# Optimization experiments

Hardware: AMD Instinct MI355X
Metric: run time of the kernel (lower is better)

The kernel has to match this reference:

```python
import jax, jax.numpy as jnp
import numpy as np

B, N, M, D, F, H = 8, 512, 512, 512, 512, 8
D_H, F_H = D // H, F // H


def setup_inputs() -> dict:
    key = jax.random.key(0)
    ks = jax.random.split(key, 7)
    X = jax.random.normal(ks[0], (B, N, D), dtype=jnp.float32)
    V = jax.random.normal(ks[1], (B, M, F), dtype=jnp.float32)
    # learned parameters, init normal(0, 0.02) as in the torch module
    W_Q_1 = 0.02 * jax.random.normal(ks[2], (H, N, D_H, D_H), dtype=jnp.float32)
    W_Q_2 = 0.02 * jax.random.normal(ks[3], (H, N, M, D_H), dtype=jnp.float32)
    W_V = 0.02 * jax.random.normal(ks[4], (H, F_H, F_H), dtype=jnp.float32)
    O_w = 0.02 * jax.random.normal(ks[5], (F, F), dtype=jnp.float32)
    O_b = jnp.zeros((F,), dtype=jnp.float32)
    return {"X": X, "V": V, "W_Q_1": W_Q_1, "W_Q_2": W_Q_2,
            "W_V": W_V, "O_w": O_w, "O_b": O_b}


def reference(X, V, W_Q_1, W_Q_2, W_V, O_w, O_b):
    b, n, d = X.shape
    _, m, f = V.shape
    Xh = X.reshape(b, n, H, d // H)      # [B,N,H,D_H]
    Vh = V.reshape(b, m, H, f // H)      # [B,M,H,F_H]
    # 'hndd' repeats d within one operand -> diagonal of W_Q_1's last two dims
    # (faithful to torch.einsum semantics): per-position per-channel scale.
    Q_1 = jnp.einsum('bnhd,hndd->bhnd', Xh, W_Q_1)
    Q_1 = jax.nn.gelu(Q_1, approximate=False)  # torch nn.GELU default = exact erf
    Q_2 = jnp.einsum('bhnd,hnmd->bhnm', Q_1, W_Q_2)  # synthesized attention logits
    A = jax.nn.softmax(Q_2, axis=3)                  # softmax over M
    # 'hff' likewise takes the diagonal of W_V -> per-head channel scale fused
    # with the attention-weighted value aggregation.
    Y = jnp.einsum('bhnm,bmhf,hff->bnhf', A, Vh, W_V)
    Y = Y.reshape(b, n, f)
    return Y @ O_w.T + O_b
```

## Files before the change

### kernel.cpp

```cpp
#include <hip/hip_runtime.h>
#include <cstdint>

#define B_ 8
#define N_ 512
#define M_ 512
#define D_ 512
#define F_ 512
#define H_ 8
#define DH_ 64
#define FH_ 64

template <int CTRL>
__device__ __forceinline__ float dpp_add(float x) {
    int y = __builtin_amdgcn_update_dpp(0, __float_as_int(x), CTRL, 0xf, 0xf, true);
    return x + __int_as_float(y);
}

__global__ __launch_bounds__(256, 4) void syn_k_attn(const float* __restrict__ X,
                                                     const float* __restrict__ W1,
                                                     const float* __restrict__ W2,
                                                     float* __restrict__ A) {
    int hn = blockIdx.x;
    int h = hn >> 9, n = hn & 511;
    int t = threadIdx.x;
    int wave = t >> 6, lane = t & 63;
    __shared__ float q1s[8 * 68];
    __shared__ float logits[8 * 520];

    {
        int d = t & 63;
        int b0 = t >> 6;
        float w = W1[(size_t)hn * (DH_ * DH_) + d * (DH_ + 1)];
        #pragma unroll
        for (int i = 0; i < 2; ++i) {
            int bi = b0 + i * 4;
            float x = X[((size_t)(bi * N_ + n)) * D_ + h * DH_ + d];
            float v = x * w;
            q1s[bi * 68 + d] = 0.5f * v * (1.0f + erff(v * 0.70710678118654752440f));
        }
    }
    __syncthreads();

    int mr = lane >> 3, c = lane & 7;
    float4 qa[8], qb[8];
    #pragma unroll
    for (int b = 0; b < 8; ++b) {
        qa[b] = *(const float4*)&q1s[b * 68 + c * 8];
        qb[b] = *(const float4*)&q1s[b * 68 + c * 8 + 4];
    }

    const float* w2 = W2 + (size_t)hn * ((size_t)M_ * DH_);
    #pragma unroll 4
    for (int g = 0; g < 16; ++g) {
        int m = (wave + g * 4) * 8 + mr;
        const float* wr = w2 + (size_t)m * DH_ + c * 8;
        float4 wa = *(const float4*)wr;
        float4 wb = *(const float4*)(wr + 4);
        float acc[8];
        #pragma unroll
        for (int b = 0; b < 8; ++b) {
            float a0 = wa.x * qa[b].x + wa.y * qa[b].y + wa.z * qa[b].z + wa.w * qa[b].w
                     + wb.x * qb[b].x + wb.y * qb[b].y + wb.z * qb[b].z + wb.w * qb[b].w;
            a0 = dpp_add<0xB1>(a0);
            a0 = dpp_add<0x4E>(a0);
            a0 = dpp_add<0x124>(a0);
            acc[b] = a0;
        }
        float lo = c == 0 ? acc[0] : c == 1 ? acc[1] : c == 2 ? acc[2] : acc[3];
        float hi = c == 0 ? acc[4] : c == 1 ? acc[5] : c == 2 ? acc[6] : acc[7];
        if (c < 4) {
            logits[c * 520 + m] = lo;
            logits[(c + 4) * 520 + m] = hi;
        }
    }
    __syncthreads();

    for (int bb = wave; bb < 8; bb += 4) {
        const float* lrow = &logits[bb * 520 + lane * 8];
        float4 va = *(const float4*)lrow;
        float4 vb = *(const float4*)(lrow + 4);
        float v[8] = {va.x, va.y, va.z, va.w, vb.x, vb.y, vb.z, vb.w};
        float mx = v[0];
        #pragma unroll
        for (int i = 1; i < 8; ++i) mx = fmaxf(mx, v[i]);
        #pragma unroll
        for (int s = 1; s < 64; s <<= 1) mx = fmaxf(mx, __shfl_xor(mx, s));
        float e[8]; float sum = 0.f;
        #pragma unroll
        for (int i = 0; i < 8; ++i) { e[i] = expf(v[i] - mx); sum += e[i]; }
        #pragma unroll
        for (int s = 1; s < 64; s <<= 1) sum += __shfl_xor(sum, s);
        float inv = 1.0f / sum;
        float* outp = A + ((size_t)(bb * H_ + h) * N_ + n) * M_ + lane * 8;
        float4 o0 = make_float4(e[0] * inv, e[1] * inv, e[2] * inv, e[3] * inv);
        float4 o1 = make_float4(e[4] * inv, e[5] * inv, e[6] * inv, e[7] * inv);
        *(float4*)outp = o0;
        *(float4*)(outp + 4) = o1;
    }
}


__global__ __launch_bounds__(256) void syn_k_pv(const float* __restrict__ A,
                                                const float* __restrict__ V,
                                                const float* __restrict__ WV,
                                                float* __restrict__ Y) {
    int bh = blockIdx.y;
    int b = bh >> 3, h = bh & 7;
    int n0 = blockIdx.x * 64;
    int t = threadIdx.x;
    int tx = t & 15, ty = t >> 4;
    __shared__ float Alds[64 * 64];
    __shared__ float Vlds[64 * 64];
    float acc[4][4] = {};
    const float* Abase = A + ((size_t)bh * N_ + n0) * M_;
    const float* Vbase = V + (size_t)b * ((size_t)M_ * F_) + h * FH_;
    int kk = tx * 4;
    for (int m0 = 0; m0 < M_; m0 += 64) {
        #pragma unroll
        for (int it = 0; it < 4; ++it) {
            int r = ty + it * 16;
            float4 a4 = *(const float4*)(Abase + (size_t)r * M_ + m0 + kk);
            int slot = ((r >> 2) ^ tx) & 15;
            float* p = &Alds[kk * 64 + slot * 4 + (r & 3)];
            p[0] = a4.x; p[64] = a4.y; p[128] = a4.z; p[192] = a4.w;
            float4 v4 = *(const float4*)(Vbase + (size_t)(m0 + r) * F_ + kk);
            *(float4*)&Vlds[r * 64 + kk] = v4;
        }
        __syncthreads();
        #pragma unroll 2
        for (int k4 = 0; k4 < 16; ++k4) {
            int sa = ((ty ^ k4) & 15) * 4;
            #pragma unroll
            for (int kj = 0; kj < 4; ++kj) {
                int k = k4 * 4 + kj;
                float4 a4 = *(const float4*)&Alds[k * 64 + sa];
                float4 v4 = *(const float4*)&Vlds[k * 64 + tx * 4];
                float ar[4] = {a4.x, a4.y, a4.z, a4.w};
                float vr[4] = {v4.x, v4.y, v4.z, v4.w};
                #pragma unroll
                for (int i = 0; i < 4; ++i)
                    #pragma unroll
                    for (int j = 0; j < 4; ++j)
                        acc[i][j] += ar[i] * vr[j];
            }
        }
        __syncthreads();
    }
    float s_[4];
    #pragma unroll
    for (int j = 0; j < 4; ++j)
        s_[j] = WV[(size_t)h * (FH_ * FH_) + (tx * 4 + j) * (FH_ + 1)];
    #pragma unroll
    for (int i = 0; i < 4; ++i) {
        int row = n0 + ty * 4 + i;
        float4 o = make_float4(acc[i][0] * s_[0], acc[i][1] * s_[1],
                               acc[i][2] * s_[2], acc[i][3] * s_[3]);
        *(float4*)(Y + ((size_t)(b * N_ + row)) * F_ + h * FH_ + tx * 4) = o;
    }
}

__global__ __launch_bounds__(256) void syn_k_out(const float* __restrict__ Yg,
                                                 const float* __restrict__ Ow,
                                                 const float* __restrict__ Ob,
                                                 float* __restrict__ out) {
    int r0 = blockIdx.y * 64;
    int f0 = blockIdx.x * 64;
    int t = threadIdx.x;
    int tx = t & 15, ty = t >> 4;
    __shared__ float Ylds[64 * 68];
    __shared__ float Wlds[64 * 64];
    float acc[4][4] = {};
    int kk = tx * 4;
    for (int k0 = 0; k0 < F_; k0 += 64) {
        #pragma unroll
        for (int it = 0; it < 4; ++it) {
            int r = ty + it * 16;
            float4 y4 = *(const float4*)(Yg + (size_t)(r0 + r) * F_ + k0 + kk);
            *(float4*)&Ylds[r * 68 + kk] = y4;
            int sl = ((r >> 2) ^ tx) & 15;
            float4 w4 = *(const float4*)(Ow + (size_t)(f0 + r) * F_ + k0 + kk);
            float* pw = &Wlds[kk * 64 + sl * 4 + (r & 3)];
            pw[0] = w4.x; pw[64] = w4.y; pw[128] = w4.z; pw[192] = w4.w;
        }
        __syncthreads();
        #pragma unroll 2
        for (int k4 = 0; k4 < 16; ++k4) {
            int sw = ((tx ^ k4) & 15) * 4;
            float ya[4][4];
            #pragma unroll
            for (int i = 0; i < 4; ++i) {
                float4 y4 = *(const float4*)&Ylds[(ty * 4 + i) * 68 + k4 * 4];
                ya[i][0] = y4.x; ya[i][1] = y4.y; ya[i][2] = y4.z; ya[i][3] = y4.w;
            }
            #pragma unroll
            for (int kj = 0; kj < 4; ++kj) {
                float4 w4 = *(const float4*)&Wlds[(k4 * 4 + kj) * 64 + sw];
                float wr[4] = {w4.x, w4.y, w4.z, w4.w};
                #pragma unroll
                for (int i = 0; i < 4; ++i)
                    #pragma unroll
                    for (int j = 0; j < 4; ++j)
                        acc[i][j] += ya[i][kj] * wr[j];
            }
        }
        __syncthreads();
    }
    float bb[4];
    #pragma unroll
    for (int j = 0; j < 4; ++j) bb[j] = Ob[f0 + tx * 4 + j];
    #pragma unroll
    for (int i = 0; i < 4; ++i) {
        int row = r0 + ty * 4 + i;
        float4 o = make_float4(acc[i][0] + bb[0], acc[i][1] + bb[1],
                               acc[i][2] + bb[2], acc[i][3] + bb[3]);
        *(float4*)(out + (size_t)row * F_ + f0 + tx * 4) = o;
    }
}

extern "C" void kernel_launch(void* const* d_in, const int* in_sizes, int n_in,
                              void* d_out, int out_size, void* d_ws, size_t ws_size,
                              hipStream_t stream) {
    const float* X  = (const float*)d_in[0];
    const float* V  = (const float*)d_in[1];
    const float* W1 = (const float*)d_in[2];
    const float* W2 = (const float*)d_in[3];
    const float* WV = (const float*)d_in[4];
    const float* Ow = (const float*)d_in[5];
    const float* Ob = (const float*)d_in[6];
    float* out = (float*)d_out;

    float* ws = (float*)d_ws;
    float* A  = ws;
    float* Y  = A + (size_t)B_ * H_ * N_ * M_;

    syn_k_attn<<<H_ * N_, 256, 0, stream>>>(X, W1, W2, A);
    syn_k_pv<<<dim3(N_ / 64, B_ * H_), 256, 0, stream>>>(A, V, WV, Y);
    syn_k_out<<<dim3(F_ / 64, (B_ * N_) / 64), 256, 0, stream>>>(Y, Ow, Ob, out);
}
```

Measured before the change: 207.0 us.

## Run output projection on bf16 MFMA using hi/lo split-precision emulation

The fp32 output projection GEMM is replaced by a bf16 MFMA kernel. It emulates fp32 accuracy with three products (hi*hi, hi*lo, lo*hi). The PV kernel now writes Y as separate bf16 high and low halves, and a new small kernel splits O_w the same way on every call. This aims to cut the FMA-bound cost of the 4096x512x512 GEMM, at the price of an extra launch, three passes over K, and slightly reduced precision.

```diff
diff --git a/kernel.cpp b/kernel.cpp
--- a/kernel.cpp
+++ b/kernel.cpp
@@ -9,6 +9,17 @@
 #define H_ 8
 #define DH_ 64
 #define FH_ 64
+
+typedef __attribute__((ext_vector_type(8))) short bf16x8;
+typedef __attribute__((ext_vector_type(4))) float f32x4;
+
+__device__ __forceinline__ unsigned short f2bf(float x) {
+    unsigned u = __float_as_uint(x);
+    return (unsigned short)((u + 0x7fffu + ((u >> 16) & 1u)) >> 16);
+}
+__device__ __forceinline__ float bf2f(unsigned short b) {
+    return __uint_as_float(((unsigned)b) << 16);
+}
 
 template <int CTRL>
 __device__ __forceinline__ float dpp_add(float x) {
@@ -99,11 +110,11 @@
     }
 }
 
-
 __global__ __launch_bounds__(256) void syn_k_pv(const float* __restrict__ A,
                                                 const float* __restrict__ V,
                                                 const float* __restrict__ WV,
-                                                float* __restrict__ Y) {
+                                                unsigned short* __restrict__ Yhi,
+                                                unsigned short* __restrict__ Ylo) {
     int bh = blockIdx.y;
     int b = bh >> 3, h = bh & 7;
     int n0 = blockIdx.x * 64;
@@ -153,68 +164,127 @@
     #pragma unroll
     for (int i = 0; i < 4; ++i) {
         int row = n0 + ty * 4 + i;
-        float4 o = make_float4(acc[i][0] * s_[0], acc[i][1] * s_[1],
-                               acc[i][2] * s_[2], acc[i][3] * s_[3]);
-        *(float4*)(Y + ((size_t)(b * N_ + row)) * F_ + h * FH_ + tx * 4) = o;
-    }
-}
-
-__global__ __launch_bounds__(256) void syn_k_out(const float* __restrict__ Yg,
-                                                 const float* __restrict__ Ow,
-                                                 const float* __restrict__ Ob,
-                                                 float* __restrict__ out) {
-    int r0 = blockIdx.y * 64;
-    int f0 = blockIdx.x * 64;
+        float ys[4];
+        #pragma unroll
+        for (int j = 0; j < 4; ++j) ys[j] = acc[i][j] * s_[j];
+        unsigned short hb[4], lb[4];
+        #pragma unroll
+        for (int j = 0; j < 4; ++j) {
+            hb[j] = f2bf(ys[j]);
+            lb[j] = f2bf(ys[j] - bf2f(hb[j]));
+        }
+        size_t base = ((size_t)(b * N_ + row)) * F_ + h * FH_ + tx * 4;
+        uint2 hv, lv;
+        hv.x = (unsigned)hb[0] | ((unsigned)hb[1] << 16);
+        hv.y = (unsigned)hb[2] | ((unsigned)hb[3] << 16);
+        lv.x = (unsigned)lb[0] | ((unsigned)lb[1] << 16);
+        lv.y = (unsigned)lb[2] | ((unsigned)lb[3] << 16);
+        *(uint2*)(Yhi + base) = hv;
+        *(uint2*)(Ylo + base) = lv;
+    }
+}
+
+__global__ __launch_bounds__(256) void syn_k_splitw(const float* __restrict__ Ow,
+                                                    unsigned short* __restrict__ Whi,
+                                                    unsigned short* __restrict__ Wlo) {
+    int i = (blockIdx.x * 256 + threadIdx.x) * 4;
+    float4 v = *(const float4*)(Ow + i);
+    float vv[4] = {v.x, v.y, v.z, v.w};
+    unsigned short hb[4], lb[4];
+    #pragma unroll
+    for (int j = 0; j < 4; ++j) {
+        hb[j] = f2bf(vv[j]);
+        lb[j] = f2bf(vv[j] - bf2f(hb[j]));
+    }
+    uint2 hv, lv;
+    hv.x = (unsigned)hb[0] | ((unsigned)hb[1] << 16);
+    hv.y = (unsigned)hb[2] | ((unsigned)hb[3] << 16);
+    lv.x = (unsigned)lb[0] | ((unsigned)lb[1] << 16);
+    lv.y = (unsigned)lb[2] | ((unsigned)lb[3] << 16);
+    *(uint2*)(Whi + i) = hv;
+    *(uint2*)(Wlo + i) = lv;
+}
+
+__global__ __launch_bounds__(256) void syn_k_out_mfma(const unsigned short* __restrict__ Yhi,
+                                                      const unsigned short* __restrict__ Ylo,
+                                                      const unsigned short* __restrict__ Whi,
+                                                      const unsigned short* __restrict__ Wlo,
+                                                      const float* __restrict__ Ob,
+                                                      float* __restrict__ out) {
+    int r0 = blockIdx.x * 64;
+    int f0 = blockIdx.y * 64;
     int t = threadIdx.x;
-    int tx = t & 15, ty = t >> 4;
-    __shared__ float Ylds[64 * 68];
-    __shared__ float Wlds[64 * 64];
-    float acc[4][4] = {};
-    int kk = tx * 4;
-    for (int k0 = 0; k0 < F_; k0 += 64) {
-        #pragma unroll
-        for (int it = 0; it < 4; ++it) {
-            int r = ty + it * 16;
-            float4 y4 = *(const float4*)(Yg + (size_t)(r0 + r) * F_ + k0 + kk);
-            *(float4*)&Ylds[r * 68 + kk] = y4;
-            int sl = ((r >> 2) ^ tx) & 15;
-            float4 w4 = *(const float4*)(Ow + (size_t)(f0 + r) * F_ + k0 + kk);
-            float* pw = &Wlds[kk * 64 + sl * 4 + (r & 3)];
-            pw[0] = w4.x; pw[64] = w4.y; pw[128] = w4.z; pw[192] = w4.w;
-        }
-        __syncthreads();
-        #pragma unroll 2
-        for (int k4 = 0; k4 < 16; ++k4) {
-            int sw = ((tx ^ k4) & 15) * 4;
-            float ya[4][4];
+    int lane = t & 63, wave = t >> 6;
+    int wr = wave >> 1, wc = wave & 1;
+    __shared__ __align__(16) unsigned short Al[64 * 64];
+    __shared__ __align__(16) unsigned short Bl[64 * 64];
+    f32x4 acc[2][2];
+    #pragma unroll
+    for (int i = 0; i < 2; ++i)
+        #pragma unroll
+        for (int j = 0; j < 2; ++j)
+            acc[i][j] = (f32x4){0.f, 0.f, 0.f, 0.f};
+
+    const unsigned short* Aseg[3] = {Yhi, Yhi, Ylo};
+    const unsigned short* Bseg[3] = {Whi, Wlo, Whi};
+
+    int srow = t >> 3, skg = t & 7;
+    int sslot = skg ^ (srow & 7);
+    unsigned aoff0 = srow * 64 + sslot * 8;
+    unsigned aoff1 = (srow + 32) * 64 + sslot * 8;
+
+    for (int seg = 0; seg < 3; ++seg) {
+        const unsigned short* Ag0 = Aseg[seg] + (size_t)(r0 + srow) * 512 + skg * 8;
+        const unsigned short* Ag1 = Aseg[seg] + (size_t)(r0 + srow + 32) * 512 + skg * 8;
+        const unsigned short* Bg0 = Bseg[seg] + (size_t)(f0 + srow) * 512 + skg * 8;
+        const unsigned short* Bg1 = Bseg[seg] + (size_t)(f0 + srow + 32) * 512 + skg * 8;
+        #pragma unroll 1
+        for (int kb = 0; kb < 512; kb += 64) {
+            float4 a0 = *(const float4*)(Ag0 + kb);
+            float4 a1 = *(const float4*)(Ag1 + kb);
+            float4 b0 = *(const float4*)(Bg0 + kb);
+            float4 b1 = *(const float4*)(Bg1 + kb);
+            *(float4*)&Al[aoff0] = a0;
+            *(float4*)&Al[aoff1] = a1;
+            *(float4*)&Bl[aoff0] = b0;
+            *(float4*)&Bl[aoff1] = b1;
+            __syncthreads();
             #pragma unroll
-            for (int i = 0; i < 4; ++i) {
-                float4 y4 = *(const float4*)&Ylds[(ty * 4 + i) * 68 + k4 * 4];
-                ya[i][0] = y4.x; ya[i][1] = y4.y; ya[i][2] = y4.z; ya[i][3] = y4.w;
+            for (int m = 0; m < 2; ++m) {
+                int kslot = (m * 4 + (lane >> 4)) ^ (lane & 7);
+                bf16x8 af[2], bfr[2];
+                #pragma unroll
+                for (int q = 0; q < 2; ++q) {
+                    int arow = wr * 32 + q * 16 + (lane & 15);
+                    af[q] = *(const bf16x8*)&Al[arow * 64 + kslot * 8];
+                    int brow = wc * 32 + q * 16 + (lane & 15);
+                    bfr[q] = *(const bf16x8*)&Bl[brow * 64 + kslot * 8];
+                }
+                #pragma unroll
+                for (int i = 0; i < 2; ++i)
+                    #pragma unroll
+                    for (int j = 0; j < 2; ++j)
+                        acc[i][j] = __builtin_amdgcn_mfma_f32_16x16x32_bf16(
+                            af[i], bfr[j], acc[i][j], 0, 0, 0);
             }
+            __syncthreads();
+        }
+    }
+
+    int crow = r0 + wr * 32 + (lane >> 4) * 4;
+    int ccol = f0 + wc * 32 + (lane & 15);
+    float ob0 = Ob[ccol], ob1 = Ob[ccol + 16];
+    #pragma unroll
+    for (int i = 0; i < 2; ++i)
+        #pragma unroll
+        for (int j = 0; j < 2; ++j) {
+            float obv = (j == 0) ? ob0 : ob1;
             #pragma unroll
-            for (int kj = 0; kj < 4; ++kj) {
-                float4 w4 = *(const float4*)&Wlds[(k4 * 4 + kj) * 64 + sw];
-                float wr[4] = {w4.x, w4.y, w4.z, w4.w};
-                #pragma unroll
-                for (int i = 0; i < 4; ++i)
-                    #pragma unroll
-                    for (int j = 0; j < 4; ++j)
-                        acc[i][j] += ya[i][kj] * wr[j];
+            for (int r = 0; r < 4; ++r) {
+                int row = crow + i * 16 + r;
+                out[(size_t)row * F_ + ccol + j * 16] = acc[i][j][r] + obv;
             }
         }
-        __syncthreads();
-    }
-    float bb[4];
-    #pragma unroll
-    for (int j = 0; j < 4; ++j) bb[j] = Ob[f0 + tx * 4 + j];
-    #pragma unroll
-    for (int i = 0; i < 4; ++i) {
-        int row = r0 + ty * 4 + i;
-        float4 o = make_float4(acc[i][0] + bb[0], acc[i][1] + bb[1],
-                               acc[i][2] + bb[2], acc[i][3] + bb[3]);
-        *(float4*)(out + (size_t)row * F_ + f0 + tx * 4) = o;
-    }
 }
 
 extern "C" void kernel_launch(void* const* d_in, const int* in_sizes, int n_in,
@@ -230,10 +300,14 @@
     float* out = (float*)d_out;
 
     float* ws = (float*)d_ws;
-    float* A  = ws;
-    float* Y  = A + (size_t)B_ * H_ * N_ * M_;
-
+    float* A = ws;
+    unsigned short* Yhi = (unsigned short*)(A + (size_t)B_ * H_ * N_ * M_);
+    unsigned short* Ylo = Yhi + (size_t)B_ * N_ * F_;
+    unsigned short* Whi = Ylo + (size_t)B_ * N_ * F_;
+    unsigned short* Wlo = Whi + (size_t)F_ * F_;
+
+    syn_k_splitw<<<(F_ * F_) / (256 * 4), 256, 0, stream>>>(Ow, Whi, Wlo);
     syn_k_attn<<<H_ * N_, 256, 0, stream>>>(X, W1, W2, A);
-    syn_k_pv<<<dim3(N_ / 64, B_ * H_), 256, 0, stream>>>(A, V, WV, Y);
-    syn_k_out<<<dim3(F_ / 64, (B_ * N_) / 64), 256, 0, stream>>>(Y, Ow, Ob, out);
-}
+    syn_k_pv<<<dim3(N_ / 64, B_ * H_), 256, 0, stream>>>(A, V, WV, Yhi, Ylo);
+    syn_k_out_mfma<<<dim3((B_ * N_) / 64, F_ / 64), 256, 0, stream>>>(Yhi, Ylo, Whi, Wlo, Ob, out);
+}
```

After: 200.4 us. -3.2%, faster.
